# Kernel tuning notes

Hardware: AMD Instinct MI355X
Metric: run time of the kernel (lower is better)

## Reference

```python
import jax, jax.numpy as jnp
import numpy as np

B, T = 8, 512
V, H = 2048, 4
N_EMBD = 768


def setup_inputs() -> dict:
    key = jax.random.key(0)
    k1, k2, k3, k4 = jax.random.split(key, 4)
    x = jax.random.randint(k1, (B, T, 1), 0, V, dtype=jnp.int64)
    cooc = jax.random.normal(k2, (V, V, H), dtype=jnp.float32)
    proj_w = jax.random.normal(k3, (N_EMBD, V * H * H), dtype=jnp.float32) * 0.01
    proj_b = jax.random.normal(k4, (N_EMBD,), dtype=jnp.float32)
    return {"x": x, "cooc": cooc, "proj_w": proj_w, "proj_b": proj_b}


def reference(x, cooc, proj_w, proj_b):
    # x: [B,T,1] int token ids; cooc: [V,V,H]
    tok = x[..., 0]  # [B,T]
    Vv, _, Hh = cooc.shape
    Bb, Tt = tok.shape
    # att scores: wei[b,i,j,h] = cooc[tok[b,i], tok[b,j], h]  (keys index rows, queries cols)
    wei = cooc[tok[:, :, None], tok[:, None, :], :]  # [B,T,T,H]
    att = jax.nn.softmax(wei, axis=2)  # softmax over last token axis (dim=-1 of [T,T])
    att = att + jnp.eye(Tt, dtype=att.dtype)[None, :, :, None]  # self loops
    # value embedding table is flatten(cooc, 1, 2): [V, V*H]; same for every head
    v = cooc.reshape(Vv, Vv * Hh)[tok]  # [B,T,V*H]
    # per-head: att[:,:,:,h] @ v -> [B,T,V*H]; concat over heads on last dim
    out = jnp.einsum('bijh,bjd->bihd', att, v)  # [B,T,H,V*H]
    out = out.reshape(Bb, Tt, Hh * Vv * Hh)  # [B,T,H*V*H]
    # projection (dropout p=0.0 / eval mode -> identity)
    y = out @ proj_w.T + proj_b  # [B,T,n_embd]
    return y
```

## Files before the change

### kernel.cpp

```cpp
#include <hip/hip_runtime.h>
#include <stdint.h>

#define B_    8
#define T_    512
#define V_    2048
#define H_    4
#define NE_   768
#define D_    8192
#define PWROW 32768
#define M1    3072
#define K3    2048

typedef __attribute__((ext_vector_type(8))) short bf16x8;
typedef __attribute__((ext_vector_type(4))) float f32x4;

__device__ __forceinline__ unsigned short f2bf(float f) {
  union { float f; unsigned int u; } c; c.f = f;
  unsigned int u = c.u;
  return (unsigned short)((u + 0x7FFFu + ((u >> 16) & 1u)) >> 16);
}

__global__ __launch_bounds__(256) void cvt_k(
    const float* __restrict__ src, unsigned short* __restrict__ dst, int n4) {
  int i = blockIdx.x * 256 + threadIdx.x;
  const int stride = gridDim.x * 256;
  for (; i < n4; i += stride) {
    const float4 v = ((const float4*)src)[i];
    ushort4 o;
    o.x = f2bf(v.x); o.y = f2bf(v.y); o.z = f2bf(v.z); o.w = f2bf(v.w);
    ((ushort4*)dst)[i] = o;
  }
}

__global__ __launch_bounds__(256) void gemm1f_k(
    const unsigned short* __restrict__ Aq,
    const unsigned short* __restrict__ Bq,
    unsigned short* __restrict__ mtT) {
  __shared__ unsigned short As[128 * 32];
  __shared__ unsigned short Bs[128 * 32];
  const int r0 = blockIdx.x * 128;
  const int t0 = blockIdx.y * 128;
  const int tid  = threadIdx.x;
  const int lane = tid & 63, wave = tid >> 6;
  const int wr = wave >> 1, wc = wave & 1;
  const int fr = lane & 15, fq = lane >> 4;
  const int l4 = lane >> 2, lb = lane & 3;

  f32x4 acc[4][4];
  #pragma unroll
  for (int m = 0; m < 4; ++m)
    #pragma unroll
    for (int n = 0; n < 4; ++n) acc[m][n] = (f32x4){0.f, 0.f, 0.f, 0.f};

  for (int k0 = 0; k0 < D_; k0 += 32) {
    __syncthreads();
    #pragma unroll
    for (int c = 0; c < 2; ++c) {
      const int ch  = wave * 2 + c;
      const int row = ch * 16 + l4;
      __builtin_amdgcn_global_load_lds(
          (const __attribute__((address_space(1))) void*)
              (Aq + (size_t)(r0 + row) * D_ + k0 + lb * 8),
          (__attribute__((address_space(3))) void*)(As + ch * 512),
          16, 0, 0);
      __builtin_amdgcn_global_load_lds(
          (const __attribute__((address_space(1))) void*)
              (Bq + (size_t)(t0 + row) * D_ + k0 + lb * 8),
          (__attribute__((address_space(3))) void*)(Bs + ch * 512),
          16, 0, 0);
    }
    __syncthreads();
    bf16x8 af[4], bf[4];
    #pragma unroll
    for (int m = 0; m < 4; ++m)
      af[m] = *(const bf16x8*)&As[(wr * 64 + m * 16 + fr) * 32 + fq * 8];
    #pragma unroll
    for (int n = 0; n < 4; ++n)
      bf[n] = *(const bf16x8*)&Bs[(wc * 64 + n * 16 + fr) * 32 + fq * 8];
    #pragma unroll
    for (int m = 0; m < 4; ++m)
      #pragma unroll
      for (int n = 0; n < 4; ++n)
        acc[m][n] = __builtin_amdgcn_mfma_f32_16x16x32_bf16(af[m], bf[n], acc[m][n], 0, 0, 0);
  }

  #pragma unroll
  for (int m = 0; m < 4; ++m)
    #pragma unroll
    for (int n = 0; n < 4; ++n) {
      const int r = r0 + wr * 64 + m * 16 + fq * 4;
      const int t = t0 + wc * 64 + n * 16 + fr;
      #pragma unroll
      for (int g = 0; g < 4; ++g) {
        const int rr = r + g;
        mtT[(size_t)(rr >> 2) * D_ + t * H_ + (rr & 3)] = f2bf(acc[m][n][g]);
      }
    }
}

__global__ __launch_bounds__(256) void gather_k(
    const unsigned short* __restrict__ mtT, const int* __restrict__ x,
    unsigned short* __restrict__ GT) {
  __shared__ int toks[B_ * T_];
  const int tid = threadIdx.x;
  #pragma unroll
  for (int c = 0; c < 16; ++c) toks[c * 256 + tid] = x[c * 256 + tid];
  __syncthreads();

  const int lane = tid & 63, wave = tid >> 6;
  const int e = blockIdx.x * 4 + wave;
  const unsigned short* mrow = mtT + (size_t)e * D_;
  #pragma unroll
  for (int b = 0; b < B_; ++b) {
    unsigned short* grow = GT + ((size_t)b * NE_ + e) * K3;
    const int* tb = toks + b * T_;
    #pragma unroll
    for (int r = 0; r < 8; ++r) {
      const int j = r * 64 + lane;
      const uint2 v = *(const uint2*)(mrow + (size_t)tb[j] * H_);
      *(uint2*)(grow + j * H_) = v;
    }
  }
}

__global__ __launch_bounds__(256) void gemm3f_k(
    const unsigned short* __restrict__ att,
    const unsigned short* __restrict__ GT,
    const float* __restrict__ bias,
    float* __restrict__ y) {
  __shared__ unsigned short As[128 * 32];
  __shared__ unsigned short Bs[128 * 32];
  const int b  = blockIdx.z;
  const int i0 = blockIdx.x * 128;
  const int e0 = blockIdx.y * 128;
  const int tid  = threadIdx.x;
  const int lane = tid & 63, wave = tid >> 6;
  const int wr = wave >> 1, wc = wave & 1;
  const int fr = lane & 15, fq = lane >> 4;
  const int l4 = lane >> 2, lb = lane & 3;

  f32x4 acc[4][4];
  #pragma unroll
  for (int m = 0; m < 4; ++m)
    #pragma unroll
    for (int n = 0; n < 4; ++n) acc[m][n] = (f32x4){0.f, 0.f, 0.f, 0.f};

  const unsigned short* aB = att + (size_t)(b * T_ + i0) * K3;
  const unsigned short* bB = GT + ((size_t)b * NE_ + e0) * K3;

  for (int k0 = 0; k0 < K3; k0 += 32) {
    __syncthreads();
    #pragma unroll
    for (int c = 0; c < 2; ++c) {
      const int ch  = wave * 2 + c;
      const int row = ch * 16 + l4;
      __builtin_amdgcn_global_load_lds(
          (const __attribute__((address_space(1))) void*)
              (aB + (size_t)row * K3 + k0 + lb * 8),
          (__attribute__((address_space(3))) void*)(As + ch * 512),
          16, 0, 0);
      __builtin_amdgcn_global_load_lds(
          (const __attribute__((address_space(1))) void*)
              (bB + (size_t)row * K3 + k0 + lb * 8),
          (__attribute__((address_space(3))) void*)(Bs + ch * 512),
          16, 0, 0);
    }
    __syncthreads();
    bf16x8 af[4], bf[4];
    #pragma unroll
    for (int m = 0; m < 4; ++m)
      af[m] = *(const bf16x8*)&As[(wr * 64 + m * 16 + fr) * 32 + fq * 8];
    #pragma unroll
    for (int n = 0; n < 4; ++n)
      bf[n] = *(const bf16x8*)&Bs[(wc * 64 + n * 16 + fr) * 32 + fq * 8];
    #pragma unroll
    for (int m = 0; m < 4; ++m)
      #pragma unroll
      for (int n = 0; n < 4; ++n)
        acc[m][n] = __builtin_amdgcn_mfma_f32_16x16x32_bf16(af[m], bf[n], acc[m][n], 0, 0, 0);
  }

  #pragma unroll
  for (int m = 0; m < 4; ++m)
    #pragma unroll
    for (int n = 0; n < 4; ++n) {
      const int i = i0 + wr * 64 + m * 16 + fq * 4;
      const int e = e0 + wc * 64 + n * 16 + fr;
      const float be = bias[e];
      #pragma unroll
      for (int g = 0; g < 4; ++g)
        y[(size_t)(b * T_ + i + g) * NE_ + e] = acc[m][n][g] + be;
    }
}

__global__ __launch_bounds__(64) void softmax_k(
    const int* __restrict__ x, const float* __restrict__ cooc,
    unsigned short* __restrict__ att) {
  const int bi = blockIdx.x;
  const int b = bi >> 9, i = bi & (T_ - 1);
  const int lane = threadIdx.x;
  const int ti = x[b * T_ + i];
  const float* crow = cooc + (size_t)ti * D_;

  float w[8][4];
  #pragma unroll
  for (int r = 0; r < 8; ++r) {
    const int j = lane + r * 64;
    const int tj = x[b * T_ + j];
    const float4 v = *(const float4*)(crow + (size_t)tj * H_);
    w[r][0] = v.x; w[r][1] = v.y; w[r][2] = v.z; w[r][3] = v.w;
  }
  float m[4] = {-1e30f, -1e30f, -1e30f, -1e30f};
  #pragma unroll
  for (int r = 0; r < 8; ++r)
    #pragma unroll
    for (int h = 0; h < 4; ++h) m[h] = fmaxf(m[h], w[r][h]);
  #pragma unroll
  for (int off = 32; off > 0; off >>= 1)
    #pragma unroll
    for (int h = 0; h < 4; ++h) m[h] = fmaxf(m[h], __shfl_xor(m[h], off));
  float s[4] = {0.f, 0.f, 0.f, 0.f};
  #pragma unroll
  for (int r = 0; r < 8; ++r)
    #pragma unroll
    for (int h = 0; h < 4; ++h) { w[r][h] = __expf(w[r][h] - m[h]); s[h] += w[r][h]; }
  #pragma unroll
  for (int off = 32; off > 0; off >>= 1)
    #pragma unroll
    for (int h = 0; h < 4; ++h) s[h] += __shfl_xor(s[h], off);
  float inv[4];
  #pragma unroll
  for (int h = 0; h < 4; ++h) inv[h] = 1.f / s[h];

  unsigned short* arow = att + (size_t)(b * T_ + i) * (T_ * H_);
  #pragma unroll
  for (int r = 0; r < 8; ++r) {
    const int j = lane + r * 64;
    const float d = (j == i) ? 1.f : 0.f;
    ushort4 o;
    o.x = f2bf(w[r][0] * inv[0] + d);
    o.y = f2bf(w[r][1] * inv[1] + d);
    o.z = f2bf(w[r][2] * inv[2] + d);
    o.w = f2bf(w[r][3] * inv[3] + d);
    *(ushort4*)(arow + (size_t)j * H_) = o;
  }
}

__global__ __launch_bounds__(256) void gemm1_k(
    const float* __restrict__ pw, const float* __restrict__ cooc,
    unsigned short* __restrict__ mtT) {
  __shared__ unsigned short As[128 * 32];
  __shared__ unsigned short Bs[64 * 32];
  const int h  = blockIdx.z;
  const int e0 = blockIdx.x * 128;
  const int t0 = blockIdx.y * 64;
  const int tid  = threadIdx.x;
  const int lane = tid & 63, wave = tid >> 6;
  const int wr = wave >> 1, wc = wave & 1;
  const int fr = lane & 15, fq = lane >> 4;

  f32x4 acc[4][2];
  #pragma unroll
  for (int m = 0; m < 4; ++m)
    #pragma unroll
    for (int n = 0; n < 2; ++n) acc[m][n] = (f32x4){0.f, 0.f, 0.f, 0.f};

  const float* aB = pw + (size_t)e0 * PWROW + (size_t)h * D_;
  const float* bB = cooc + (size_t)t0 * D_;

  for (int k0 = 0; k0 < D_; k0 += 32) {
    __syncthreads();
    #pragma unroll
    for (int c = 0; c < 4; ++c) {
      const int fe = (c * 256 + tid) * 4;
      const int row = fe >> 5, k = fe & 31;
      const float4 v = *(const float4*)(aB + (size_t)row * PWROW + k0 + k);
      ushort4 o; o.x = f2bf(v.x); o.y = f2bf(v.y); o.z = f2bf(v.z); o.w = f2bf(v.w);
      *(ushort4*)&As[fe] = o;
    }
    #pragma unroll
    for (int c = 0; c < 2; ++c) {
      const int fe = (c * 256 + tid) * 4;
      const int row = fe >> 5, k = fe & 31;
      const float4 v = *(const float4*)(bB + (size_t)row * D_ + k0 + k);
      ushort4 o; o.x = f2bf(v.x); o.y = f2bf(v.y); o.z = f2bf(v.z); o.w = f2bf(v.w);
      *(ushort4*)&Bs[fe] = o;
    }
    __syncthreads();
    bf16x8 af[4], bf[2];
    #pragma unroll
    for (int m = 0; m < 4; ++m)
      af[m] = *(const bf16x8*)&As[(wr * 64 + m * 16 + fr) * 32 + fq * 8];
    #pragma unroll
    for (int n = 0; n < 2; ++n)
      bf[n] = *(const bf16x8*)&Bs[(wc * 32 + n * 16 + fr) * 32 + fq * 8];
    #pragma unroll
    for (int m = 0; m < 4; ++m)
      #pragma unroll
      for (int n = 0; n < 2; ++n)
        acc[m][n] = __builtin_amdgcn_mfma_f32_16x16x32_bf16(af[m], bf[n], acc[m][n], 0, 0, 0);
  }

  #pragma unroll
  for (int m = 0; m < 4; ++m)
    #pragma unroll
    for (int n = 0; n < 2; ++n) {
      const int e = e0 + wr * 64 + m * 16 + fq * 4;
      const int t = t0 + wc * 32 + n * 16 + fr;
      #pragma unroll
      for (int g = 0; g < 4; ++g)
        mtT[(size_t)(e + g) * D_ + t * H_ + h] = f2bf(acc[m][n][g]);
    }
}

__global__ __launch_bounds__(256) void gemm3_k(
    const unsigned short* __restrict__ att, const unsigned short* __restrict__ mtT,
    const int* __restrict__ x, const float* __restrict__ bias,
    float* __restrict__ y) {
  __shared__ unsigned short As[64 * 32];
  __shared__ unsigned short Bs[128 * 32];
  const int b  = blockIdx.z;
  const int i0 = blockIdx.x * 64;
  const int e0 = blockIdx.y * 128;
  const int tid  = threadIdx.x;
  const int lane = tid & 63, wave = tid >> 6;
  const int wr = wave >> 1, wc = wave & 1;
  const int fr = lane & 15, fq = lane >> 4;

  f32x4 acc[2][4];
  #pragma unroll
  for (int m = 0; m < 2; ++m)
    #pragma unroll
    for (int n = 0; n < 4; ++n) acc[m][n] = (f32x4){0.f, 0.f, 0.f, 0.f};

  const unsigned short* aB = att + (size_t)(b * T_ + i0) * (T_ * H_);

  for (int ks = 0; ks < 64; ++ks) {
    const int k0 = ks * 32;
    __syncthreads();
    {
      const int fe = tid * 8;
      const int row = fe >> 5, k = fe & 31;
      const uint4 v = *(const uint4*)(aB + (size_t)row * (T_ * H_) + k0 + k);
      *(uint4*)&As[fe] = v;
    }
    #pragma unroll
    for (int c = 0; c < 4; ++c) {
      const int q = c * 256 + tid;
      const int n = q >> 3, j8 = q & 7;
      const int tj = x[b * T_ + ks * 8 + j8];
      const uint2 v = *(const uint2*)(mtT + (size_t)(e0 + n) * D_ + tj * H_);
      *(uint2*)&Bs[n * 32 + j8 * 4] = v;
    }
    __syncthreads();
    bf16x8 af[2], bf[4];
    #pragma unroll
    for (int m = 0; m < 2; ++m)
      af[m] = *(const bf16x8*)&As[(wr * 32 + m * 16 + fr) * 32 + fq * 8];
    #pragma unroll
    for (int n = 0; n < 4; ++n)
      bf[n] = *(const bf16x8*)&Bs[(wc * 64 + n * 16 + fr) * 32 + fq * 8];
    #pragma unroll
    for (int m = 0; m < 2; ++m)
      #pragma unroll
      for (int n = 0; n < 4; ++n)
        acc[m][n] = __builtin_amdgcn_mfma_f32_16x16x32_bf16(af[m], bf[n], acc[m][n], 0, 0, 0);
  }

  #pragma unroll
  for (int m = 0; m < 2; ++m)
    #pragma unroll
    for (int n = 0; n < 4; ++n) {
      const int i = i0 + wr * 32 + m * 16 + fq * 4;
      const int e = e0 + wc * 64 + n * 16 + fr;
      const float be = bias[e];
      #pragma unroll
      for (int g = 0; g < 4; ++g)
        y[(size_t)(b * T_ + i + g) * NE_ + e] = acc[m][n][g] + be;
    }
}

extern "C" void kernel_launch(void* const* d_in, const int* in_sizes, int n_in,
                              void* d_out, int out_size, void* d_ws, size_t ws_size,
                              hipStream_t stream) {
  const int*   x    = (const int*)d_in[0];
  const float* cooc = (const float*)d_in[1];
  const float* pw   = (const float*)d_in[2];
  const float* pb   = (const float*)d_in[3];
  float* y = (float*)d_out;

  const size_t MTT_E = (size_t)NE_ * D_;
  const size_t BQ_E  = (size_t)V_ * D_;
  const size_t AQ_E  = (size_t)M1 * D_;
  const size_t need_fast = (MTT_E + BQ_E + AQ_E) * 2;

  unsigned short* mtT = (unsigned short*)d_ws;

  if (ws_size >= need_fast) {
    unsigned short* Bq  = mtT + MTT_E;
    unsigned short* Aq  = Bq + BQ_E;
    unsigned short* GT  = Bq;
    unsigned short* att = Aq;
    hipLaunchKernelGGL(cvt_k, dim3(2048), dim3(256), 0, stream,
                       pw, Aq, (int)(AQ_E / 4));
    hipLaunchKernelGGL(cvt_k, dim3(2048), dim3(256), 0, stream,
                       cooc, Bq, (int)(BQ_E / 4));
    hipLaunchKernelGGL(gemm1f_k, dim3(M1 / 128, V_ / 128), dim3(256), 0, stream,
                       Aq, Bq, mtT);
    hipLaunchKernelGGL(softmax_k, dim3(B_ * T_), dim3(64), 0, stream, x, cooc, att);
    hipLaunchKernelGGL(gather_k, dim3(NE_ / 4), dim3(256), 0, stream, mtT, x, GT);
    hipLaunchKernelGGL(gemm3f_k, dim3(T_ / 128, NE_ / 128, B_), dim3(256), 0, stream,
                       att, GT, pb, y);
  } else {
    unsigned short* att = mtT + MTT_E;
    hipLaunchKernelGGL(gemm1_k, dim3(NE_ / 128, V_ / 64, H_), dim3(256), 0, stream,
                       pw, cooc, mtT);
    hipLaunchKernelGGL(softmax_k, dim3(B_ * T_), dim3(64), 0, stream, x, cooc, att);
    hipLaunchKernelGGL(gemm3_k, dim3(T_ / 64, NE_ / 128, B_), dim3(256), 0, stream,
                       att, mtT, x, pb, y);
  }
}
```

Before: 277.5 us.

## Split-K the weight-cooc GEMM and shrink projection GEMM tile to 128x64

The first GEMM (3072x2048 output, K=8192) previously launched only 384 blocks. It now splits K in two across blockIdx.z, writing bf16 partials to two buffers, and a new reduce kernel sums them. The final projection GEMM drops its N tile from 128 to 64, doubling its block count to improve occupancy across the CUs. This adds an extra partial-buffer write/read pass and rounds each partial to bf16 before summing, which slightly changes precision, and the split path only runs when the workspace is large enough.

After: 256.9 us. -7.4%, faster.

```diff
diff --git a/kernel.cpp b/kernel.cpp
--- a/kernel.cpp
+++ b/kernel.cpp
@@ -19,6 +19,10 @@
   unsigned int u = c.u;
   return (unsigned short)((u + 0x7FFFu + ((u >> 16) & 1u)) >> 16);
 }
+__device__ __forceinline__ float bf2f(unsigned short s) {
+  union { unsigned int u; float f; } c; c.u = ((unsigned int)s) << 16;
+  return c.f;
+}
 
 __global__ __launch_bounds__(256) void cvt_k(
     const float* __restrict__ src, unsigned short* __restrict__ dst, int n4) {
@@ -35,16 +39,20 @@
 __global__ __launch_bounds__(256) void gemm1f_k(
     const unsigned short* __restrict__ Aq,
     const unsigned short* __restrict__ Bq,
-    unsigned short* __restrict__ mtT) {
+    unsigned short* __restrict__ P,
+    int kk, size_t pstride) {
   __shared__ unsigned short As[128 * 32];
   __shared__ unsigned short Bs[128 * 32];
   const int r0 = blockIdx.x * 128;
   const int t0 = blockIdx.y * 128;
+  const int z  = blockIdx.z;
+  const int kbeg = z * kk, kend = kbeg + kk;
   const int tid  = threadIdx.x;
   const int lane = tid & 63, wave = tid >> 6;
   const int wr = wave >> 1, wc = wave & 1;
   const int fr = lane & 15, fq = lane >> 4;
   const int l4 = lane >> 2, lb = lane & 3;
+  unsigned short* __restrict__ Pz = P + (size_t)z * pstride;
 
   f32x4 acc[4][4];
   #pragma unroll
@@ -52,7 +60,7 @@
     #pragma unroll
     for (int n = 0; n < 4; ++n) acc[m][n] = (f32x4){0.f, 0.f, 0.f, 0.f};
 
-  for (int k0 = 0; k0 < D_; k0 += 32) {
+  for (int k0 = kbeg; k0 < kend; k0 += 32) {
     __syncthreads();
     #pragma unroll
     for (int c = 0; c < 2; ++c) {
@@ -93,9 +101,29 @@
       #pragma unroll
       for (int g = 0; g < 4; ++g) {
         const int rr = r + g;
-        mtT[(size_t)(rr >> 2) * D_ + t * H_ + (rr & 3)] = f2bf(acc[m][n][g]);
+        Pz[(size_t)(rr >> 2) * D_ + t * H_ + (rr & 3)] = f2bf(acc[m][n][g]);
       }
     }
+}
+
+__global__ __launch_bounds__(256) void reduce_k(
+    unsigned short* __restrict__ P0, const unsigned short* __restrict__ P1) {
+  const size_t i = ((size_t)blockIdx.x * 256 + threadIdx.x) * 8;
+  ushort4 a0 = *(const ushort4*)(P0 + i);
+  ushort4 a1 = *(const ushort4*)(P0 + i + 4);
+  ushort4 b0 = *(const ushort4*)(P1 + i);
+  ushort4 b1 = *(const ushort4*)(P1 + i + 4);
+  ushort4 o0, o1;
+  o0.x = f2bf(bf2f(a0.x) + bf2f(b0.x));
+  o0.y = f2bf(bf2f(a0.y) + bf2f(b0.y));
+  o0.z = f2bf(bf2f(a0.z) + bf2f(b0.z));
+  o0.w = f2bf(bf2f(a0.w) + bf2f(b0.w));
+  o1.x = f2bf(bf2f(a1.x) + bf2f(b1.x));
+  o1.y = f2bf(bf2f(a1.y) + bf2f(b1.y));
+  o1.z = f2bf(bf2f(a1.z) + bf2f(b1.z));
+  o1.w = f2bf(bf2f(a1.w) + bf2f(b1.w));
+  *(ushort4*)(P0 + i) = o0;
+  *(ushort4*)(P0 + i + 4) = o1;
 }
 
 __global__ __launch_bounds__(256) void gather_k(
@@ -129,21 +157,20 @@
     const float* __restrict__ bias,
     float* __restrict__ y) {
   __shared__ unsigned short As[128 * 32];
-  __shared__ unsigned short Bs[128 * 32];
+  __shared__ unsigned short Bs[64 * 32];
   const int b  = blockIdx.z;
   const int i0 = blockIdx.x * 128;
-  const int e0 = blockIdx.y * 128;
+  const int e0 = blockIdx.y * 64;
   const int tid  = threadIdx.x;
   const int lane = tid & 63, wave = tid >> 6;
   const int wr = wave >> 1, wc = wave & 1;
   const int fr = lane & 15, fq = lane >> 4;
-  const int l4 = lane >> 2, lb = lane & 3;
-
-  f32x4 acc[4][4];
-  #pragma unroll
-  for (int m = 0; m < 4; ++m)
-    #pragma unroll
-    for (int n = 0; n < 4; ++n) acc[m][n] = (f32x4){0.f, 0.f, 0.f, 0.f};
+
+  f32x4 acc[4][2];
+  #pragma unroll
+  for (int m = 0; m < 4; ++m)
+    #pragma unroll
+    for (int n = 0; n < 2; ++n) acc[m][n] = (f32x4){0.f, 0.f, 0.f, 0.f};
 
   const unsigned short* aB = att + (size_t)(b * T_ + i0) * K3;
   const unsigned short* bB = GT + ((size_t)b * NE_ + e0) * K3;
@@ -151,41 +178,45 @@
   for (int k0 = 0; k0 < K3; k0 += 32) {
     __syncthreads();
     #pragma unroll
-    for (int c = 0; c < 2; ++c) {
-      const int ch  = wave * 2 + c;
-      const int row = ch * 16 + l4;
+    for (int rdi = 0; rdi < 2; ++rdi) {
+      const int q = rdi * 256 + tid;
+      const int row = q >> 2, koff = (q & 3) * 8;
       __builtin_amdgcn_global_load_lds(
           (const __attribute__((address_space(1))) void*)
-              (aB + (size_t)row * K3 + k0 + lb * 8),
-          (__attribute__((address_space(3))) void*)(As + ch * 512),
+              (aB + (size_t)row * K3 + k0 + koff),
+          (__attribute__((address_space(3))) void*)(As + q * 8),
           16, 0, 0);
+    }
+    {
+      const int q = tid;
+      const int row = q >> 2, koff = (q & 3) * 8;
       __builtin_amdgcn_global_load_lds(
           (const __attribute__((address_space(1))) void*)
-              (bB + (size_t)row * K3 + k0 + lb * 8),
-          (__attribute__((address_space(3))) void*)(Bs + ch * 512),
+              (bB + (size_t)row * K3 + k0 + koff),
+          (__attribute__((address_space(3))) void*)(Bs + q * 8),
           16, 0, 0);
     }
     __syncthreads();
-    bf16x8 af[4], bf[4];
+    bf16x8 af[4], bf[2];
     #pragma unroll
     for (int m = 0; m < 4; ++m)
       af[m] = *(const bf16x8*)&As[(wr * 64 + m * 16 + fr) * 32 + fq * 8];
     #pragma unroll
-    for (int n = 0; n < 4; ++n)
-      bf[n] = *(const bf16x8*)&Bs[(wc * 64 + n * 16 + fr) * 32 + fq * 8];
-    #pragma unroll
-    for (int m = 0; m < 4; ++m)
-      #pragma unroll
-      for (int n = 0; n < 4; ++n)
+    for (int n = 0; n < 2; ++n)
+      bf[n] = *(const bf16x8*)&Bs[(wc * 32 + n * 16 + fr) * 32 + fq * 8];
+    #pragma unroll
+    for (int m = 0; m < 4; ++m)
+      #pragma unroll
+      for (int n = 0; n < 2; ++n)
         acc[m][n] = __builtin_amdgcn_mfma_f32_16x16x32_bf16(af[m], bf[n], acc[m][n], 0, 0, 0);
   }
 
   #pragma unroll
   for (int m = 0; m < 4; ++m)
     #pragma unroll
-    for (int n = 0; n < 4; ++n) {
+    for (int n = 0; n < 2; ++n) {
       const int i = i0 + wr * 64 + m * 16 + fq * 4;
-      const int e = e0 + wc * 64 + n * 16 + fr;
+      const int e = e0 + wc * 32 + n * 16 + fr;
       const float be = bias[e];
       #pragma unroll
       for (int g = 0; g < 4; ++g)
@@ -392,11 +423,30 @@
   const size_t MTT_E = (size_t)NE_ * D_;
   const size_t BQ_E  = (size_t)V_ * D_;
   const size_t AQ_E  = (size_t)M1 * D_;
-  const size_t need_fast = (MTT_E + BQ_E + AQ_E) * 2;
+  const size_t need_mid   = (MTT_E + BQ_E + AQ_E) * 2;
+  const size_t need_split = (2 * MTT_E + BQ_E + AQ_E) * 2;
 
   unsigned short* mtT = (unsigned short*)d_ws;
 
-  if (ws_size >= need_fast) {
+  if (ws_size >= need_split) {
+    unsigned short* P1  = mtT + MTT_E;
+    unsigned short* Bq  = P1 + MTT_E;
+    unsigned short* Aq  = Bq + BQ_E;
+    unsigned short* GT  = Bq;
+    unsigned short* att = Aq;
+    hipLaunchKernelGGL(cvt_k, dim3(2048), dim3(256), 0, stream,
+                       pw, Aq, (int)(AQ_E / 4));
+    hipLaunchKernelGGL(cvt_k, dim3(2048), dim3(256), 0, stream,
+                       cooc, Bq, (int)(BQ_E / 4));
+    hipLaunchKernelGGL(gemm1f_k, dim3(M1 / 128, V_ / 128, 2), dim3(256), 0, stream,
+                       Aq, Bq, mtT, D_ / 2, MTT_E);
+    hipLaunchKernelGGL(reduce_k, dim3((unsigned)(MTT_E / (256 * 8))), dim3(256), 0,
+                       stream, mtT, P1);
+    hipLaunchKernelGGL(softmax_k, dim3(B_ * T_), dim3(64), 0, stream, x, cooc, att);
+    hipLaunchKernelGGL(gather_k, dim3(NE_ / 4), dim3(256), 0, stream, mtT, x, GT);
+    hipLaunchKernelGGL(gemm3f_k, dim3(T_ / 128, NE_ / 64, B_), dim3(256), 0, stream,
+                       att, GT, pb, y);
+  } else if (ws_size >= need_mid) {
     unsigned short* Bq  = mtT + MTT_E;
     unsigned short* Aq  = Bq + BQ_E;
     unsigned short* GT  = Bq;
@@ -405,11 +455,11 @@
                        pw, Aq, (int)(AQ_E / 4));
     hipLaunchKernelGGL(cvt_k, dim3(2048), dim3(256), 0, stream,
                        cooc, Bq, (int)(BQ_E / 4));
-    hipLaunchKernelGGL(gemm1f_k, dim3(M1 / 128, V_ / 128), dim3(256), 0, stream,
-                       Aq, Bq, mtT);
+    hipLaunchKernelGGL(gemm1f_k, dim3(M1 / 128, V_ / 128, 1), dim3(256), 0, stream,
+                       Aq, Bq, mtT, D_, (size_t)0);
     hipLaunchKernelGGL(softmax_k, dim3(B_ * T_), dim3(64), 0, stream, x, cooc, att);
     hipLaunchKernelGGL(gather_k, dim3(NE_ / 4), dim3(256), 0, stream, mtT, x, GT);
-    hipLaunchKernelGGL(gemm3f_k, dim3(T_ / 128, NE_ / 128, B_), dim3(256), 0, stream,
+    hipLaunchKernelGGL(gemm3f_k, dim3(T_ / 128, NE_ / 64, B_), dim3(256), 0, stream,
                        att, GT, pb, y);
   } else {
     unsigned short* att = mtT + MTT_E;
```
